# Kernel tuning notes

Hardware: AMD Instinct MI355X
Metric: run time of the kernel (lower is better)

The kernel has to match this reference:

```python
import jax, jax.numpy as jnp
import numpy as np

P_LEN, Q_LEN, BATCH, D, H = 300, 50, 32, 256, 256


def _make_params(key):
    ks = jax.random.split(key, 6)
    s = lambda k, shape, fan: jax.random.normal(k, shape, jnp.float32) * (1.0 / np.sqrt(fan))
    return dict(
        Wq=s(ks[0], (2, H, D), D), bq=jnp.zeros((2, H), jnp.float32),
        Wp=s(ks[1], (2, H, D), D), bp=jnp.zeros((2, H), jnp.float32),
        Wr=s(ks[2], (2, H, H), H), br=jnp.zeros((2, H), jnp.float32),
        Wg=s(ks[3], (2, H), H), bg=jnp.zeros((2,), jnp.float32),
        ln_g=jnp.ones((2, 2 * D), jnp.float32), ln_b=jnp.zeros((2, 2 * D), jnp.float32),
        W_ih=s(ks[4], (2, 4 * H, 2 * D), 2 * D), W_hh=s(ks[5], (2, 4 * H, H), H),
        b_ih=jnp.zeros((2, 4 * H), jnp.float32), b_hh=jnp.zeros((2, 4 * H), jnp.float32),
    )


def setup_inputs() -> dict:
    key = jax.random.key(0)
    k1, k2, k3, k4, kp = jax.random.split(key, 5)
    content_vec = jax.random.normal(k1, (P_LEN, BATCH, D), jnp.float32)
    question_vec = jax.random.normal(k2, (Q_LEN, BATCH, D), jnp.float32)
    p_len = jax.random.randint(k3, (BATCH,), P_LEN // 2, P_LEN + 1)
    q_len = jax.random.randint(k4, (BATCH,), Q_LEN // 2, Q_LEN + 1)
    content_mask = (jnp.arange(P_LEN)[None, :] < p_len[:, None]).astype(jnp.int32)
    question_mask = (jnp.arange(Q_LEN)[None, :] < q_len[:, None]).astype(jnp.int32)
    inp = dict(content_vec=content_vec, content_mask=content_mask,
               question_vec=question_vec, question_mask=question_mask)
    inp.update(_make_params(kp))
    return inp


def _masked_flip(v, mask):
    # v: (P, B, D); mask: (B, P). Reverses the valid prefix of each sequence,
    # leaving padding positions in place (standard Match-LSTM masked_flip).
    P = v.shape[0]
    lengths = mask.sum(axis=1)  # (B,)
    t = jnp.arange(P)[:, None]  # (P, 1)
    idx = jnp.where(t < lengths[None, :], lengths[None, :] - 1 - t, t)  # (P, B)
    idx = jnp.broadcast_to(idx[:, :, None], v.shape)
    return jnp.take_along_axis(v, idx, axis=0)


def _uni_match(cv, qv, qmask, Wq, bq, Wp, bp, Wr, br, Wg, bg, ln_g, ln_b, W_ih, W_hh, b_ih, b_hh):
    # cv: (P, B, D), qv: (Q, B, D), qmask: (B, Q)
    B = cv.shape[1]
    Hh = Wr.shape[0]
    wh = jnp.einsum('qbd,hd->qbh', qv, Wq) + bq      # (Q, B, H), precomputed once
    hp_all = jnp.einsum('pbd,hd->pbh', cv, Wp) + bp  # (P, B, H), precomputed
    pad = (qmask == 0)                               # (B, Q)

    def step(carry, xs):
        h, c = carry
        cv_t, hp_t = xs
        hr = h @ Wr.T + br                                    # (B, H)
        g = jnp.tanh(wh + hp_t[None] + hr[None])              # (Q, B, H)
        alpha = (jnp.einsum('qbh,h->qb', g, Wg) + bg).T       # (B, Q)
        alpha = jax.nn.softmax(jnp.where(pad, -jnp.inf, alpha), axis=1)
        h_alpha = jnp.einsum('bq,qbd->bd', alpha, qv)         # (B, D)
        z = jnp.concatenate([cv_t, h_alpha], axis=1)          # (B, 2D)
        mu = jnp.mean(z, axis=-1, keepdims=True)
        var = jnp.mean((z - mu) ** 2, axis=-1, keepdims=True)
        z = (z - mu) * jax.lax.rsqrt(var + 1e-5) * ln_g + ln_b
        gates = z @ W_ih.T + b_ih + h @ W_hh.T + b_hh         # (B, 4H)
        i_, f_, g_, o_ = jnp.split(gates, 4, axis=1)          # torch LSTMCell order i,f,g,o
        c_n = jax.nn.sigmoid(f_) * c + jax.nn.sigmoid(i_) * jnp.tanh(g_)
        h_n = jax.nn.sigmoid(o_) * jnp.tanh(c_n)
        return (h_n, c_n), h_n

    h0 = jnp.zeros((B, Hh), cv.dtype)
    _, hs = jax.lax.scan(step, (h0, h0), (cv, hp_all))
    return hs  # (P, B, H)


def reference(content_vec, content_mask, question_vec, question_mask,
              Wq, bq, Wp, bp, Wr, br, Wg, bg, ln_g, ln_b, W_ih, W_hh, b_ih, b_hh):
    # Dropout with p=0 (inference) is identity.
    args = lambda i: (Wq[i], bq[i], Wp[i], bp[i], Wr[i], br[i], Wg[i], bg[i],
                      ln_g[i], ln_b[i], W_ih[i], W_hh[i], b_ih[i], b_hh[i])
    right = _uni_match(content_vec, question_vec, question_mask, *args(0))
    cv_flip = _masked_flip(content_vec, content_mask)
    left = _uni_match(cv_flip, question_vec, question_mask, *args(1))
    left = _masked_flip(left, content_mask)
    res = jnp.concatenate([right, left], axis=2)            # (P, B, 2H)
    return content_mask.T[:, :, None].astype(res.dtype) * res
```

## Files before the change

### kernel.cpp

```cpp
#include <hip/hip_runtime.h>
#include <hip/hip_fp16.h>

typedef unsigned int u32;
typedef _Float16 half2_t __attribute__((ext_vector_type(2)));

static constexpr int PL = 300;
static constexpr int QL = 50;
static constexpr int B  = 32;
static constexpr int D  = 256;
static constexpr int H  = 256;

__device__ __forceinline__ float fdot2(u32 w, u32 x, float acc) {
    return __builtin_amdgcn_fdot2(__builtin_bit_cast(half2_t, w),
                                  __builtin_bit_cast(half2_t, x), acc, false);
}

__global__ __launch_bounds__(256) void pack256(const float* __restrict__ W,
                                               u32* __restrict__ dst) {
    int id = blockIdx.x * 256 + threadIdx.x;
    int g  = id >> 15;
    int r  = id & 32767;
    int kc = r >> 10;
    int j  = (r >> 2) & 255;
    int w  = r & 3;
    int k  = kc * 8 + w * 2;
    const float* s = &W[(g * 256 + j) * 256 + k];
    half2_t h2; h2[0] = (_Float16)s[0]; h2[1] = (_Float16)s[1];
    dst[id] = __builtin_bit_cast(u32, h2);
}

__global__ __launch_bounds__(256) void packWc(const float* __restrict__ Wih,
                                              const float* __restrict__ Whh,
                                              u32* __restrict__ dst) {
    int id = blockIdx.x * 256 + threadIdx.x;
    int g  = id / 393216;
    int r  = id % 393216;
    int kc = r >> 12;
    int j  = (r >> 2) & 1023;
    int w  = r & 3;
    int k  = kc * 8 + w * 2;
    float a, bb;
    if (k < 512) { const float* s = &Wih[(g * 1024 + j) * 512 + k];         a = s[0]; bb = s[1]; }
    else         { const float* s = &Whh[(g * 1024 + j) * 256 + (k - 512)]; a = s[0]; bb = s[1]; }
    half2_t h2; h2[0] = (_Float16)a; h2[1] = (_Float16)bb;
    dst[id] = __builtin_bit_cast(u32, h2);
}

__global__ __launch_bounds__(256) void prep_proj(const float* __restrict__ X,
                                                 const float* __restrict__ W,
                                                 const float* __restrict__ Bv,
                                                 __half* __restrict__ out,
                                                 int T, int nt) {
    int id = blockIdx.x;
    int tb = id % nt; id /= nt;
    int b  = id % B;  id /= B;
    int g  = id;
    int t0 = tb * 8;
    int nr = T - t0; if (nr > 8) nr = 8;
    __shared__ __align__(16) float xs[8][256];
    int tid = threadIdx.x;
    for (int r = 0; r < nr; r++) xs[r][tid] = X[((t0 + r) * B + b) * D + tid];
    __syncthreads();
    const float4* wrow = (const float4*)&W[(g * H + tid) * D];
    float bb = Bv[g * H + tid];
    float acc[8];
#pragma unroll
    for (int r = 0; r < 8; r++) acc[r] = bb;
    for (int d4 = 0; d4 < D / 4; d4++) {
        float4 w = wrow[d4];
#pragma unroll
        for (int r = 0; r < 8; r++) {
            float4 x = *(const float4*)&xs[r][d4 * 4];
            acc[r] = fmaf(w.x, x.x, fmaf(w.y, x.y, fmaf(w.z, x.z, fmaf(w.w, x.w, acc[r]))));
        }
    }
    for (int r = 0; r < nr; r++)
        out[((g * B + b) * T + t0 + r) * H + tid] = __float2half(acc[r]);
}

__global__ __launch_bounds__(512) void scan_k(
    const float* __restrict__ cv,
    const int*   __restrict__ cmask,
    const float* __restrict__ qv,
    const int*   __restrict__ qmask,
    const float* __restrict__ Wgv,
    const float* __restrict__ bgv,
    const float* __restrict__ lngp,
    const float* __restrict__ lnbp,
    const float* __restrict__ brp,
    const float* __restrict__ bih,
    const float* __restrict__ bhh,
    const u32*   __restrict__ Wr4,
    const u32*   __restrict__ Wc4,
    const __half* __restrict__ whp,
    const __half* __restrict__ hpp,
    float* __restrict__ out)
{
    int wg = blockIdx.x;
    int g = wg >> 5, b = wg & 31;
    int tid  = threadIdx.x;
    int lane = tid & 63, wave = tid >> 6;

    __shared__ __align__(16) u32  sh_whu[6400];
    __shared__ __align__(16) u32  sh_qvu[6400];
    __shared__ __align__(16) u32  sh_x[384];
    __shared__ __align__(16) float sh_zf[512];
    __shared__ float sh_g[1024];
    __shared__ float sh_h[256];
    __shared__ float sh_c[256];
    __shared__ float sh_hrA[256];
    __shared__ float sh_hrB[256];
    __shared__ float sh_alpha[64];
    __shared__ float sh_red[20];
    __shared__ int   sh_len;

    const u32* whsrc = (const u32*)(whp + (size_t)(g * B + b) * QL * H);
    for (int i = tid; i < 6400; i += 512) sh_whu[i] = whsrc[i];
    for (int i = tid; i < 6400; i += 512) {
        int q = i >> 7, d2 = i & 127;
        float2 v = *(const float2*)&qv[(q * B + b) * D + d2 * 2];
        half2_t h2; h2[0] = (_Float16)v.x; h2[1] = (_Float16)v.y;
        sh_qvu[i] = __builtin_bit_cast(u32, h2);
    }
    if (tid < 256) { sh_h[tid] = 0.f; sh_c[tid] = 0.f; }
    if (wave == 0) {
        int s = 0;
        for (int t = lane; t < PL; t += 64) s += cmask[b * PL + t];
#pragma unroll
        for (int m = 32; m; m >>= 1) s += __shfl_xor(s, m, 64);
        if (lane == 0) sh_len = s;
    }
    __syncthreads();
    int len = sh_len;
    for (int i = tid; i < (PL - len) * 256; i += 512) {
        int t = len + (i >> 8), ch = i & 255;
        out[(t * B + b) * 512 + g * 256 + ch] = 0.f;
    }

    float wgr[4];
#pragma unroll
    for (int i = 0; i < 4; i++) wgr[i] = Wgv[g * H + lane + i * 64];
    float bgs = bgv[g];
    float bias1 = bih[g * 1024 + tid]       + bhh[g * 1024 + tid];
    float bias2 = bih[g * 1024 + 512 + tid] + bhh[g * 1024 + 512 + tid];
    float2 lng = {0.f, 0.f}, lnb = {0.f, 0.f};
    float brv = 0.f;
    if (tid < 256) {
        lng = *(const float2*)&lngp[g * 512 + 2 * tid];
        lnb = *(const float2*)&lnbp[g * 512 + 2 * tid];
        brv = brp[g * H + tid];
    }
    const uint4* wrq = (const uint4*)Wr4 + (size_t)g * 8192;
    const uint4* wcq = (const uint4*)Wc4 + (size_t)g * (96 * 1024);
    const __half* hpb = hpp + (size_t)(g * B + b) * PL * H;

    for (int t = 0; t < len; t++) {
        int t_src = g ? (len - 1 - t) : t;

        if (tid < 256) {
            sh_zf[tid] = cv[(t_src * B + b) * D + tid];
        } else if (tid >= 384) {
            int i = tid - 384;
            half2_t h2; h2[0] = (_Float16)sh_h[2 * i]; h2[1] = (_Float16)sh_h[2 * i + 1];
            sh_x[256 + i] = __builtin_bit_cast(u32, h2);
        }
        __syncthreads();

        {
            int s = tid >> 8, h = tid & 255;
            float acc = s ? 0.f : brv;
            const uint4* wr = wrq + h;
#pragma unroll 4
            for (int kc = s * 16; kc < s * 16 + 16; kc++) {
                uint4 xw = *(const uint4*)&sh_x[256 + kc * 4];
                uint4 ww = wr[kc * 256];
                acc = fdot2(ww.x, xw.x, acc);
                acc = fdot2(ww.y, xw.y, acc);
                acc = fdot2(ww.z, xw.z, acc);
                acc = fdot2(ww.w, xw.w, acc);
            }
            (s ? sh_hrB : sh_hrA)[h] = acc;
        }
        __syncthreads();

        {
            const __half* hp_row = hpb + (size_t)t_src * H;
            float rp[4];
#pragma unroll
            for (int i = 0; i < 4; i++) {
                int h = lane + i * 64;
                rp[i] = sh_hrA[h] + sh_hrB[h] + (float)hp_row[h];
            }
            const __half* whh = (const __half*)sh_whu;
            for (int q = wave; q < QL; q += 8) {
                float a = 0.f;
#pragma unroll
                for (int i = 0; i < 4; i++) {
                    int h = lane + i * 64;
                    float x = (float)whh[q * H + h] + rp[i];
                    float e = __expf(2.f * x);
                    float th = (e - 1.f) / (e + 1.f);
                    a = fmaf(wgr[i], th, a);
                }
#pragma unroll
                for (int m = 32; m; m >>= 1) a += __shfl_xor(a, m, 64);
                if (lane == 0)
                    sh_alpha[q] = (qmask[b * QL + q] == 0) ? -1e30f : (a + bgs);
            }
        }
        __syncthreads();

        if (wave == 0) {
            float v = (lane < QL) ? sh_alpha[lane] : -1e30f;
            float m = v;
#pragma unroll
            for (int s = 32; s; s >>= 1) m = fmaxf(m, __shfl_xor(m, s, 64));
            float e = (lane < QL) ? __expf(v - m) : 0.f;
            float sum = e;
#pragma unroll
            for (int s = 32; s; s >>= 1) sum += __shfl_xor(sum, s, 64);
            if (lane < QL) sh_alpha[lane] = e / sum;
        }
        __syncthreads();

        if (tid < 256) {
            const __half* qvh = (const __half*)sh_qvu;
            float s = 0.f;
            for (int q = 0; q < QL; q++)
                s = fmaf(sh_alpha[q], (float)qvh[q * H + tid], s);
            sh_zf[256 + tid] = s;
        }
        __syncthreads();

        {
            float v = sh_zf[tid];
            float sx = v, sxx = v * v;
#pragma unroll
            for (int s = 32; s; s >>= 1) { sx += __shfl_xor(sx, s, 64); sxx += __shfl_xor(sxx, s, 64); }
            if (lane == 0) { sh_red[wave * 2] = sx; sh_red[wave * 2 + 1] = sxx; }
        }
        __syncthreads();
        if (tid == 0) {
            float s = 0.f, ss = 0.f;
#pragma unroll
            for (int w = 0; w < 8; w++) { s += sh_red[2 * w]; ss += sh_red[2 * w + 1]; }
            float mu = s * (1.f / 512.f);
            float var = ss * (1.f / 512.f) - mu * mu;
            sh_red[16] = mu; sh_red[17] = rsqrtf(var + 1e-5f);
        }
        __syncthreads();
        if (tid < 256) {
            float mu = sh_red[16], rs = sh_red[17];
            float2 z = *(const float2*)&sh_zf[2 * tid];
            float z0 = (z.x - mu) * rs * lng.x + lnb.x;
            float z1 = (z.y - mu) * rs * lng.y + lnb.y;
            half2_t h2; h2[0] = (_Float16)z0; h2[1] = (_Float16)z1;
            sh_x[tid] = __builtin_bit_cast(u32, h2);
        }
        __syncthreads();

        {
            float a1 = bias1, a2 = bias2;
#pragma unroll 2
            for (int kc = 0; kc < 96; kc++) {
                uint4 xw = *(const uint4*)&sh_x[kc * 4];
                uint4 w1 = wcq[kc * 1024 + tid];
                uint4 w2 = wcq[kc * 1024 + 512 + tid];
                a1 = fdot2(w1.x, xw.x, a1); a1 = fdot2(w1.y, xw.y, a1);
                a1 = fdot2(w1.z, xw.z, a1); a1 = fdot2(w1.w, xw.w, a1);
                a2 = fdot2(w2.x, xw.x, a2); a2 = fdot2(w2.y, xw.y, a2);
                a2 = fdot2(w2.z, xw.z, a2); a2 = fdot2(w2.w, xw.w, a2);
            }
            sh_g[tid] = a1; sh_g[512 + tid] = a2;
        }
        __syncthreads();

        if (tid < 256) {
            float iv = sh_g[tid], fv = sh_g[256 + tid], gv = sh_g[512 + tid], ov = sh_g[768 + tid];
            float si = 1.f / (1.f + __expf(-iv));
            float sf = 1.f / (1.f + __expf(-fv));
            float so = 1.f / (1.f + __expf(-ov));
            float eg = __expf(2.f * gv); float tg = (eg - 1.f) / (eg + 1.f);
            float c = sf * sh_c[tid] + si * tg;
            float ec = __expf(2.f * c); float tc = (ec - 1.f) / (ec + 1.f);
            float hv = so * tc;
            sh_c[tid] = c; sh_h[tid] = hv;
            out[(t_src * B + b) * 512 + g * 256 + tid] = hv;
        }
        __syncthreads();
    }
}

extern "C" void kernel_launch(void* const* d_in, const int* in_sizes, int n_in,
                              void* d_out, int out_size, void* d_ws, size_t ws_size,
                              hipStream_t stream) {
    const float* cv    = (const float*)d_in[0];
    const int*   cmask = (const int*)  d_in[1];
    const float* qv    = (const float*)d_in[2];
    const int*   qmask = (const int*)  d_in[3];
    const float* Wq    = (const float*)d_in[4];
    const float* bq    = (const float*)d_in[5];
    const float* Wp    = (const float*)d_in[6];
    const float* bp    = (const float*)d_in[7];
    const float* Wr    = (const float*)d_in[8];
    const float* br    = (const float*)d_in[9];
    const float* Wg    = (const float*)d_in[10];
    const float* bg    = (const float*)d_in[11];
    const float* ln_g  = (const float*)d_in[12];
    const float* ln_b  = (const float*)d_in[13];
    const float* Wih   = (const float*)d_in[14];
    const float* Whh   = (const float*)d_in[15];
    const float* b_ih  = (const float*)d_in[16];
    const float* b_hh  = (const float*)d_in[17];
    float* out = (float*)d_out;

    uint8_t* ws = (uint8_t*)d_ws;
    u32*    Wr4 = (u32*)ws;    ws += (size_t)2 * 32 * 256 * 4 * 4;
    u32*    Wc4 = (u32*)ws;    ws += (size_t)2 * 96 * 1024 * 4 * 4;
    __half* whp = (__half*)ws; ws += (size_t)2 * 32 * 50 * 256 * 2;
    __half* hpp = (__half*)ws;

    hipLaunchKernelGGL(pack256, dim3(256), dim3(256), 0, stream, Wr, Wr4);
    hipLaunchKernelGGL(packWc, dim3(3072), dim3(256), 0, stream, Wih, Whh, Wc4);
    hipLaunchKernelGGL(prep_proj, dim3(2 * 32 * 7), dim3(256), 0, stream,
                       qv, Wq, bq, whp, QL, 7);
    hipLaunchKernelGGL(prep_proj, dim3(2 * 32 * 38), dim3(256), 0, stream,
                       cv, Wp, bp, hpp, PL, 38);
    hipLaunchKernelGGL(scan_k, dim3(64), dim3(512), 0, stream,
                       cv, cmask, qv, qmask, Wg, bg, ln_g, ln_b, br, b_ih, b_hh,
                       Wr4, Wc4, whp, hpp, out);
}
```

Measured before the change: 5.020 ms.

## Split each recurrent chain across four cooperating blocks with register-resident LSTM weights

The scan is split from 64 blocks to 256. Four blocks now cooperate on each (direction, batch) chain, and each owns 64 hidden units. Each block keeps its slice of the LSTM gate weights in registers and its slice of Wr in LDS, so the per-step global weight streaming goes away. The blocks swap hidden state and partial Wr·h products through global memory, guarded by release/acquire flags and double-buffered. This costs a cross-block spin-wait every step, and it relies on all 256 blocks being co-resident, otherwise it deadlocks.

```diff
diff --git a/kernel.cpp b/kernel.cpp
--- a/kernel.cpp
+++ b/kernel.cpp
@@ -13,6 +13,10 @@
 __device__ __forceinline__ float fdot2(u32 w, u32 x, float acc) {
     return __builtin_amdgcn_fdot2(__builtin_bit_cast(half2_t, w),
                                   __builtin_bit_cast(half2_t, x), acc, false);
+}
+__device__ __forceinline__ u32 packh2(float a, float b) {
+    half2_t h2; h2[0] = (_Float16)a; h2[1] = (_Float16)b;
+    return __builtin_bit_cast(u32, h2);
 }
 
 __global__ __launch_bounds__(256) void pack256(const float* __restrict__ W,
@@ -25,8 +29,7 @@
     int w  = r & 3;
     int k  = kc * 8 + w * 2;
     const float* s = &W[(g * 256 + j) * 256 + k];
-    half2_t h2; h2[0] = (_Float16)s[0]; h2[1] = (_Float16)s[1];
-    dst[id] = __builtin_bit_cast(u32, h2);
+    dst[id] = packh2(s[0], s[1]);
 }
 
 __global__ __launch_bounds__(256) void packWc(const float* __restrict__ Wih,
@@ -42,8 +45,7 @@
     float a, bb;
     if (k < 512) { const float* s = &Wih[(g * 1024 + j) * 512 + k];         a = s[0]; bb = s[1]; }
     else         { const float* s = &Whh[(g * 1024 + j) * 256 + (k - 512)]; a = s[0]; bb = s[1]; }
-    half2_t h2; h2[0] = (_Float16)a; h2[1] = (_Float16)bb;
-    dst[id] = __builtin_bit_cast(u32, h2);
+    dst[id] = packh2(a, bb);
 }
 
 __global__ __launch_bounds__(256) void prep_proj(const float* __restrict__ X,
@@ -78,7 +80,7 @@
         out[((g * B + b) * T + t0 + r) * H + tid] = __float2half(acc[r]);
 }
 
-__global__ __launch_bounds__(512) void scan_k(
+__global__ __launch_bounds__(256, 1) void scan2(
     const float* __restrict__ cv,
     const int*   __restrict__ cmask,
     const float* __restrict__ qv,
@@ -94,35 +96,65 @@
     const u32*   __restrict__ Wc4,
     const __half* __restrict__ whp,
     const __half* __restrict__ hpp,
+    float*       __restrict__ exch_h,
+    float*       __restrict__ exch_hrp,
+    u32*         __restrict__ flags,
     float* __restrict__ out)
 {
-    int wg = blockIdx.x;
-    int g = wg >> 5, b = wg & 31;
+    int blk = blockIdx.x;
+    int k0  = blk >> 6;
+    int cid = blk & 63;
+    int g = cid >> 5, b = cid & 31;
     int tid  = threadIdx.x;
     int lane = tid & 63, wave = tid >> 6;
 
-    __shared__ __align__(16) u32  sh_whu[6400];
-    __shared__ __align__(16) u32  sh_qvu[6400];
+    __shared__ __align__(16) u32  sh_wh[6400];
+    __shared__ __align__(16) u32  sh_W2[8192];
     __shared__ __align__(16) u32  sh_x[384];
-    __shared__ __align__(16) float sh_zf[512];
-    __shared__ float sh_g[1024];
-    __shared__ float sh_h[256];
-    __shared__ float sh_c[256];
-    __shared__ float sh_hrA[256];
-    __shared__ float sh_hrB[256];
+    __shared__ float sh_g[256];
+    __shared__ float sh_hr[256];
+    __shared__ u32   sh_hm2[32];
+    __shared__ u32   sh_al2[32];
     __shared__ float sh_alpha[64];
-    __shared__ float sh_red[20];
+    __shared__ float sh_red[16];
+    __shared__ float sh_qb[64];
     __shared__ int   sh_len;
 
-    const u32* whsrc = (const u32*)(whp + (size_t)(g * B + b) * QL * H);
-    for (int i = tid; i < 6400; i += 512) sh_whu[i] = whsrc[i];
-    for (int i = tid; i < 6400; i += 512) {
-        int q = i >> 7, d2 = i & 127;
-        float2 v = *(const float2*)&qv[(q * B + b) * D + d2 * 2];
-        half2_t h2; h2[0] = (_Float16)v.x; h2[1] = (_Float16)v.y;
-        sh_qvu[i] = __builtin_bit_cast(u32, h2);
-    }
-    if (tid < 256) { sh_h[tid] = 0.f; sh_c[tid] = 0.f; }
+    uint4 wreg[96];
+    u32   qvreg[25];
+    int row = wave * 256 + k0 * 64 + (tid & 63);
+
+    {
+        const uint4* wcq = (const uint4*)Wc4 + (size_t)g * 96 * 1024;
+#pragma unroll
+        for (int kc = 0; kc < 96; kc++) wreg[kc] = wcq[kc * 1024 + row];
+    }
+#pragma unroll
+    for (int q2 = 0; q2 < 25; q2++) {
+        float a  = qv[(2 * q2) * (B * D) + b * D + tid];
+        float bb = qv[(2 * q2 + 1) * (B * D) + b * D + tid];
+        qvreg[q2] = packh2(a, bb);
+    }
+    {
+        const u32* whsrc = (const u32*)(whp + (size_t)(g * B + b) * QL * H);
+        for (int i = tid; i < 6400; i += 256) sh_wh[i] = whsrc[i];
+    }
+#pragma unroll
+    for (int j2 = 0; j2 < 32; j2++) {
+        int kc = 8 * k0 + (j2 >> 2), w = j2 & 3;
+        sh_W2[j2 * 256 + tid] = Wr4[((size_t)(g * 32 + kc) * 256 + tid) * 4 + w];
+    }
+    if (tid < 64) sh_qb[tid] = (tid < QL) ? (qmask[b * QL + tid] ? 0.f : -1e30f) : -1e30f;
+
+    float wgr[4];
+#pragma unroll
+    for (int i = 0; i < 4; i++) wgr[i] = Wgv[g * H + (tid & 63) + i * 64];
+    float bgs   = bgv[g];
+    float bias_g = bih[g * 1024 + row] + bhh[g * 1024 + row];
+    float lng0 = lngp[g * 512 + tid], lng1 = lngp[g * 512 + 256 + tid];
+    float lnb0 = lnbp[g * 512 + tid], lnb1 = lnbp[g * 512 + 256 + tid];
+    float brv  = brp[g * H + tid];
+
     if (wave == 0) {
         int s = 0;
         for (int t = lane; t < PL; t += 64) s += cmask[b * PL + t];
@@ -130,82 +162,74 @@
         for (int m = 32; m; m >>= 1) s += __shfl_xor(s, m, 64);
         if (lane == 0) sh_len = s;
     }
+    if (tid < 32) sh_hm2[tid] = 0;
     __syncthreads();
     int len = sh_len;
-    for (int i = tid; i < (PL - len) * 256; i += 512) {
-        int t = len + (i >> 8), ch = i & 255;
-        out[(t * B + b) * 512 + g * 256 + ch] = 0.f;
-    }
-
-    float wgr[4];
-#pragma unroll
-    for (int i = 0; i < 4; i++) wgr[i] = Wgv[g * H + lane + i * 64];
-    float bgs = bgv[g];
-    float bias1 = bih[g * 1024 + tid]       + bhh[g * 1024 + tid];
-    float bias2 = bih[g * 1024 + 512 + tid] + bhh[g * 1024 + 512 + tid];
-    float2 lng = {0.f, 0.f}, lnb = {0.f, 0.f};
-    float brv = 0.f;
-    if (tid < 256) {
-        lng = *(const float2*)&lngp[g * 512 + 2 * tid];
-        lnb = *(const float2*)&lnbp[g * 512 + 2 * tid];
-        brv = brp[g * H + tid];
-    }
-    const uint4* wrq = (const uint4*)Wr4 + (size_t)g * 8192;
-    const uint4* wcq = (const uint4*)Wc4 + (size_t)g * (96 * 1024);
+
+    for (int i = tid; i < (PL - len) * 64; i += 256) {
+        int t = len + (i >> 6), j = i & 63;
+        out[(t * B + b) * 512 + g * 256 + k0 * 64 + j] = 0.f;
+    }
+
+    u32* my_flag = &flags[(cid * 4 + k0) * 16];
+
+    {
+        float* eh0  = exch_h   + ((0 * 64 + cid) * 4 + k0) * 64;
+        float* ehr0 = exch_hrp + ((0 * 64 + cid) * 4 + k0) * 256;
+        if (tid < 64) eh0[tid] = 0.f;
+        ehr0[tid] = 0.f;
+    }
+    __threadfence();
+    __syncthreads();
+    if (tid == 0)
+        __hip_atomic_store(my_flag, 1u, __ATOMIC_RELEASE, __HIP_MEMORY_SCOPE_AGENT);
+
+    float c_reg = 0.f;
     const __half* hpb = hpp + (size_t)(g * B + b) * PL * H;
 
     for (int t = 0; t < len; t++) {
         int t_src = g ? (len - 1 - t) : t;
 
-        if (tid < 256) {
-            sh_zf[tid] = cv[(t_src * B + b) * D + tid];
-        } else if (tid >= 384) {
-            int i = tid - 384;
-            half2_t h2; h2[0] = (_Float16)sh_h[2 * i]; h2[1] = (_Float16)sh_h[2 * i + 1];
-            sh_x[256 + i] = __builtin_bit_cast(u32, h2);
-        }
-        __syncthreads();
-
-        {
-            int s = tid >> 8, h = tid & 255;
-            float acc = s ? 0.f : brv;
-            const uint4* wr = wrq + h;
-#pragma unroll 4
-            for (int kc = s * 16; kc < s * 16 + 16; kc++) {
-                uint4 xw = *(const uint4*)&sh_x[256 + kc * 4];
-                uint4 ww = wr[kc * 256];
-                acc = fdot2(ww.x, xw.x, acc);
-                acc = fdot2(ww.y, xw.y, acc);
-                acc = fdot2(ww.z, xw.z, acc);
-                acc = fdot2(ww.w, xw.w, acc);
-            }
-            (s ? sh_hrB : sh_hrA)[h] = acc;
-        }
-        __syncthreads();
-
-        {
-            const __half* hp_row = hpb + (size_t)t_src * H;
-            float rp[4];
-#pragma unroll
-            for (int i = 0; i < 4; i++) {
-                int h = lane + i * 64;
-                rp[i] = sh_hrA[h] + sh_hrB[h] + (float)hp_row[h];
-            }
-            const __half* whh = (const __half*)sh_whu;
-            for (int q = wave; q < QL; q += 8) {
+        float cvv = cv[(t_src * B + b) * D + tid];
+        float hpv = (float)hpb[(size_t)t_src * H + tid];
+
+        if (wave == 0 && lane < 4 && lane != k0) {
+            const u32* fl = &flags[(cid * 4 + lane) * 16];
+            while (__hip_atomic_load(fl, __ATOMIC_ACQUIRE, __HIP_MEMORY_SCOPE_AGENT)
+                   < (u32)(t + 1))
+                __builtin_amdgcn_s_sleep(1);
+        }
+        __syncthreads();
+        __threadfence();
+
+        {
+            const float* eh  = exch_h   + ((t & 1) * 64 + cid) * 4 * 64;
+            const float* ehr = exch_hrp + ((t & 1) * 64 + cid) * 4 * 256;
+            float hrs = ehr[tid] + ehr[256 + tid] + ehr[512 + tid] + ehr[768 + tid];
+            sh_hr[tid] = hrs + brv + hpv;
+            float hval = eh[tid];
+            float ho = __shfl_xor(hval, 1, 64);
+            if (!(tid & 1)) sh_x[256 + (tid >> 1)] = packh2(hval, ho);
+        }
+        __syncthreads();
+
+        {
+            float hrv[4];
+#pragma unroll
+            for (int i = 0; i < 4; i++) hrv[i] = sh_hr[(tid & 63) + 64 * i];
+            const __half* wh16 = (const __half*)sh_wh;
+            for (int q = wave; q < QL; q += 4) {
                 float a = 0.f;
 #pragma unroll
                 for (int i = 0; i < 4; i++) {
-                    int h = lane + i * 64;
-                    float x = (float)whh[q * H + h] + rp[i];
+                    float x = (float)wh16[q * H + (tid & 63) + 64 * i] + hrv[i];
                     float e = __expf(2.f * x);
                     float th = (e - 1.f) / (e + 1.f);
                     a = fmaf(wgr[i], th, a);
                 }
 #pragma unroll
                 for (int m = 32; m; m >>= 1) a += __shfl_xor(a, m, 64);
-                if (lane == 0)
-                    sh_alpha[q] = (qmask[b * QL + q] == 0) ? -1e30f : (a + bgs);
+                if (lane == 0) sh_alpha[q] = a + bgs + sh_qb[q];
             }
         }
         __syncthreads();
@@ -219,75 +243,98 @@
             float sum = e;
 #pragma unroll
             for (int s = 32; s; s >>= 1) sum += __shfl_xor(sum, s, 64);
-            if (lane < QL) sh_alpha[lane] = e / sum;
-        }
-        __syncthreads();
-
-        if (tid < 256) {
-            const __half* qvh = (const __half*)sh_qvu;
-            float s = 0.f;
-            for (int q = 0; q < QL; q++)
-                s = fmaf(sh_alpha[q], (float)qvh[q * H + tid], s);
-            sh_zf[256 + tid] = s;
-        }
-        __syncthreads();
-
-        {
-            float v = sh_zf[tid];
-            float sx = v, sxx = v * v;
-#pragma unroll
-            for (int s = 32; s; s >>= 1) { sx += __shfl_xor(sx, s, 64); sxx += __shfl_xor(sxx, s, 64); }
-            if (lane == 0) { sh_red[wave * 2] = sx; sh_red[wave * 2 + 1] = sxx; }
-        }
-        __syncthreads();
-        if (tid == 0) {
-            float s = 0.f, ss = 0.f;
-#pragma unroll
-            for (int w = 0; w < 8; w++) { s += sh_red[2 * w]; ss += sh_red[2 * w + 1]; }
+            float al = e / sum;
+            float alo = __shfl_xor(al, 1, 64);
+            if (lane < QL && !(lane & 1)) sh_al2[lane >> 1] = packh2(al, alo);
+        }
+        __syncthreads();
+
+        {
+            float ha0 = 0.f, ha1 = 0.f;
+#pragma unroll
+            for (int q2 = 0; q2 < 25; q2 += 2) ha0 = fdot2(qvreg[q2], sh_al2[q2], ha0);
+#pragma unroll
+            for (int q2 = 1; q2 < 25; q2 += 2) ha1 = fdot2(qvreg[q2], sh_al2[q2], ha1);
+            float z0 = cvv, z1 = ha0 + ha1;
+            float sx = z0 + z1, sxx = z0 * z0 + z1 * z1;
+#pragma unroll
+            for (int s = 32; s; s >>= 1) {
+                sx  += __shfl_xor(sx, s, 64);
+                sxx += __shfl_xor(sxx, s, 64);
+            }
+            if (lane == 0) { sh_red[wave] = sx; sh_red[8 + wave] = sxx; }
+            __syncthreads();
+            float s  = sh_red[0] + sh_red[1] + sh_red[2] + sh_red[3];
+            float ss = sh_red[8] + sh_red[9] + sh_red[10] + sh_red[11];
             float mu = s * (1.f / 512.f);
-            float var = ss * (1.f / 512.f) - mu * mu;
-            sh_red[16] = mu; sh_red[17] = rsqrtf(var + 1e-5f);
-        }
-        __syncthreads();
-        if (tid < 256) {
-            float mu = sh_red[16], rs = sh_red[17];
-            float2 z = *(const float2*)&sh_zf[2 * tid];
-            float z0 = (z.x - mu) * rs * lng.x + lnb.x;
-            float z1 = (z.y - mu) * rs * lng.y + lnb.y;
-            half2_t h2; h2[0] = (_Float16)z0; h2[1] = (_Float16)z1;
-            sh_x[tid] = __builtin_bit_cast(u32, h2);
-        }
-        __syncthreads();
-
-        {
-            float a1 = bias1, a2 = bias2;
-#pragma unroll 2
-            for (int kc = 0; kc < 96; kc++) {
-                uint4 xw = *(const uint4*)&sh_x[kc * 4];
-                uint4 w1 = wcq[kc * 1024 + tid];
-                uint4 w2 = wcq[kc * 1024 + 512 + tid];
-                a1 = fdot2(w1.x, xw.x, a1); a1 = fdot2(w1.y, xw.y, a1);
-                a1 = fdot2(w1.z, xw.z, a1); a1 = fdot2(w1.w, xw.w, a1);
-                a2 = fdot2(w2.x, xw.x, a2); a2 = fdot2(w2.y, xw.y, a2);
-                a2 = fdot2(w2.z, xw.z, a2); a2 = fdot2(w2.w, xw.w, a2);
+            float rs = rsqrtf(ss * (1.f / 512.f) - mu * mu + 1e-5f);
+            float z0n = (z0 - mu) * rs * lng0 + lnb0;
+            float z1n = (z1 - mu) * rs * lng1 + lnb1;
+            float o0 = __shfl_xor(z0n, 1, 64);
+            float o1 = __shfl_xor(z1n, 1, 64);
+            int m2 = tid >> 1;
+            if (!(tid & 1)) sh_x[m2] = packh2(z0n, o0);
+            else            sh_x[128 + m2] = packh2(o1, z1n);
+        }
+        __syncthreads();
+
+        {
+            float a0 = bias_g, a1 = 0.f, a2 = 0.f, a3 = 0.f;
+#pragma unroll
+            for (int kc = 0; kc < 96; kc += 4) {
+                uint4 x0 = *(const uint4*)&sh_x[(kc + 0) * 4];
+                uint4 w0 = wreg[kc + 0];
+                a0 = fdot2(w0.x, x0.x, a0); a0 = fdot2(w0.y, x0.y, a0);
+                a0 = fdot2(w0.z, x0.z, a0); a0 = fdot2(w0.w, x0.w, a0);
+                uint4 x1 = *(const uint4*)&sh_x[(kc + 1) * 4];
+                uint4 w1 = wreg[kc + 1];
+                a1 = fdot2(w1.x, x1.x, a1); a1 = fdot2(w1.y, x1.y, a1);
+                a1 = fdot2(w1.z, x1.z, a1); a1 = fdot2(w1.w, x1.w, a1);
+                uint4 x2 = *(const uint4*)&sh_x[(kc + 2) * 4];
+                uint4 w2 = wreg[kc + 2];
+                a2 = fdot2(w2.x, x2.x, a2); a2 = fdot2(w2.y, x2.y, a2);
+                a2 = fdot2(w2.z, x2.z, a2); a2 = fdot2(w2.w, x2.w, a2);
+                uint4 x3 = *(const uint4*)&sh_x[(kc + 3) * 4];
+                uint4 w3 = wreg[kc + 3];
+                a3 = fdot2(w3.x, x3.x, a3); a3 = fdot2(w3.y, x3.y, a3);
+                a3 = fdot2(w3.z, x3.z, a3); a3 = fdot2(w3.w, x3.w, a3);
             }
-            sh_g[tid] = a1; sh_g[512 + tid] = a2;
-        }
-        __syncthreads();
-
-        if (tid < 256) {
-            float iv = sh_g[tid], fv = sh_g[256 + tid], gv = sh_g[512 + tid], ov = sh_g[768 + tid];
+            sh_g[tid] = (a0 + a1) + (a2 + a3);
+        }
+        __syncthreads();
+
+        float* eh_w  = exch_h   + (((t + 1) & 1) * 64 + cid) * 4 * 64  + k0 * 64;
+        float* ehr_w = exch_hrp + (((t + 1) & 1) * 64 + cid) * 4 * 256 + k0 * 256;
+        if (tid < 64) {
+            float iv = sh_g[tid], fv = sh_g[64 + tid], gv = sh_g[128 + tid], ov = sh_g[192 + tid];
             float si = 1.f / (1.f + __expf(-iv));
             float sf = 1.f / (1.f + __expf(-fv));
             float so = 1.f / (1.f + __expf(-ov));
             float eg = __expf(2.f * gv); float tg = (eg - 1.f) / (eg + 1.f);
-            float c = sf * sh_c[tid] + si * tg;
+            float c = sf * c_reg + si * tg;
             float ec = __expf(2.f * c); float tc = (ec - 1.f) / (ec + 1.f);
             float hv = so * tc;
-            sh_c[tid] = c; sh_h[tid] = hv;
-            out[(t_src * B + b) * 512 + g * 256 + tid] = hv;
-        }
-        __syncthreads();
+            c_reg = c;
+            out[(t_src * B + b) * 512 + g * 256 + k0 * 64 + tid] = hv;
+            eh_w[tid] = hv;
+            float ho = __shfl_xor(hv, 1, 64);
+            if (!(tid & 1)) sh_hm2[tid >> 1] = packh2(hv, ho);
+        }
+        __syncthreads();
+
+        {
+            float p0 = 0.f, p1 = 0.f;
+#pragma unroll
+            for (int j2 = 0; j2 < 32; j2 += 2) p0 = fdot2(sh_W2[j2 * 256 + tid], sh_hm2[j2], p0);
+#pragma unroll
+            for (int j2 = 1; j2 < 32; j2 += 2) p1 = fdot2(sh_W2[j2 * 256 + tid], sh_hm2[j2], p1);
+            ehr_w[tid] = p0 + p1;
+        }
+        __threadfence();
+        __syncthreads();
+        if (tid == 0)
+            __hip_atomic_store(my_flag, (u32)(t + 2),
+                               __ATOMIC_RELEASE, __HIP_MEMORY_SCOPE_AGENT);
     }
 }
 
@@ -318,15 +365,19 @@
     u32*    Wr4 = (u32*)ws;    ws += (size_t)2 * 32 * 256 * 4 * 4;
     u32*    Wc4 = (u32*)ws;    ws += (size_t)2 * 96 * 1024 * 4 * 4;
     __half* whp = (__half*)ws; ws += (size_t)2 * 32 * 50 * 256 * 2;
-    __half* hpp = (__half*)ws;
-
+    __half* hpp = (__half*)ws; ws += (size_t)2 * 32 * 300 * 256 * 2;
+    float* exch_h   = (float*)ws; ws += (size_t)2 * 64 * 4 * 64 * 4;
+    float* exch_hrp = (float*)ws; ws += (size_t)2 * 64 * 4 * 256 * 4;
+    u32*   flags    = (u32*)ws;
+
+    hipMemsetAsync(flags, 0, (size_t)64 * 4 * 16 * 4, stream);
     hipLaunchKernelGGL(pack256, dim3(256), dim3(256), 0, stream, Wr, Wr4);
     hipLaunchKernelGGL(packWc, dim3(3072), dim3(256), 0, stream, Wih, Whh, Wc4);
     hipLaunchKernelGGL(prep_proj, dim3(2 * 32 * 7), dim3(256), 0, stream,
                        qv, Wq, bq, whp, QL, 7);
     hipLaunchKernelGGL(prep_proj, dim3(2 * 32 * 38), dim3(256), 0, stream,
                        cv, Wp, bp, hpp, PL, 38);
-    hipLaunchKernelGGL(scan_k, dim3(64), dim3(512), 0, stream,
+    hipLaunchKernelGGL(scan2, dim3(256), dim3(256), 0, stream,
                        cv, cmask, qv, qmask, Wg, bg, ln_g, ln_b, br, b_ih, b_hh,
-                       Wr4, Wc4, whp, hpp, out);
-}
+                       Wr4, Wc4, whp, hpp, exch_h, exch_hrp, flags, out);
+}
```

Result: slower. 12.79 ms (+154.8%).
